# Optimization experiments

Hardware: AMD Instinct MI355X
Metric: run time of the kernel (lower is better)

Reference implementation:

```python
import jax, jax.numpy as jnp
import numpy as np

N_NODES = 100000
N_FEAT = 512
N_CLASS = 64
N_EDGES = 3200000
NLAYERS = 2


def setup_inputs() -> dict:
    key = jax.random.key(0)
    k1, k2, k3, k4, k5 = jax.random.split(key, 5)
    x = jax.random.normal(k1, (N_NODES, N_FEAT), dtype=jnp.float32)
    # xavier_uniform on weight.T => bound = sqrt(6/(fan_in+fan_out))
    bound = float(np.sqrt(6.0 / (N_FEAT + N_CLASS)))
    weight = jax.random.uniform(k2, (N_FEAT, N_CLASS), dtype=jnp.float32,
                                minval=-bound, maxval=bound)
    bias = jnp.zeros((N_CLASS,), dtype=jnp.float32)
    edge_row = jax.random.randint(k3, (N_EDGES,), 0, N_NODES, dtype=jnp.int32)
    edge_col = jax.random.randint(k4, (N_EDGES,), 0, N_NODES, dtype=jnp.int32)
    edge_val = jax.random.uniform(k5, (N_EDGES,), dtype=jnp.float32)
    return {"x": x, "weight": weight, "bias": bias,
            "edge_row": edge_row, "edge_col": edge_col, "edge_val": edge_val,
            "nlayers": NLAYERS}


def _spmm(edge_row, edge_col, edge_val, h):
    # out[r] = sum_{e: row[e]==r} val[e] * h[col[e]]   (adj @ h)
    msgs = edge_val[:, None] * h[edge_col]  # [E, C]
    return jax.ops.segment_sum(msgs, edge_row, num_segments=h.shape[0])


def reference(x, weight, bias, edge_row, edge_col, edge_val, nlayers):
    h = x @ weight                      # [N, C] dense GEMM
    for _ in range(nlayers):            # repeated sparse propagation
        h = _spmm(edge_row, edge_col, edge_val, h)
    h = h + bias
    return jax.nn.log_softmax(h, axis=1)
```

## Files before the change

### kernel.cpp

```cpp
#include <hip/hip_runtime.h>
#include <hip/hip_bf16.h>

constexpr int NROWS = 100000;
constexpr int K     = 512;
constexpr int C     = 64;
constexpr int E     = 3200000;

constexpr int NBK     = 256;
constexpr int BROWS   = 391;
constexpr int BSTRIDE = 13824;
constexpr int CHUNK   = 4096;

__global__ __launch_bounds__(256) void gemm64(const float* __restrict__ x,
                                              const float* __restrict__ w,
                                              float* __restrict__ h) {
  __shared__ float xs[128][65];
  __shared__ float ws[64][64];
  const int t    = threadIdx.x;
  const int cg   = (t & 15) * 4;
  const int rg   = (t >> 4) * 8;
  const int row0 = blockIdx.x * 128;

  float acc[8][4] = {};

  for (int k0 = 0; k0 < K; k0 += 64) {
    {
      const float4* wg  = (const float4*)(w + (size_t)k0 * C);
      float4*       wsv = (float4*)&ws[0][0];
#pragma unroll
      for (int i = 0; i < 4; ++i) wsv[t + 256 * i] = wg[t + 256 * i];
    }
#pragma unroll
    for (int i = 0; i < 8; ++i) {
      int idx = t + 256 * i;
      int r   = idx >> 4;
      int kk  = (idx & 15) * 4;
      int gr  = row0 + r;
      if (gr >= NROWS) gr = NROWS - 1;
      float4 v = *(const float4*)(x + (size_t)gr * K + k0 + kk);
      xs[r][kk]     = v.x;
      xs[r][kk + 1] = v.y;
      xs[r][kk + 2] = v.z;
      xs[r][kk + 3] = v.w;
    }
    __syncthreads();

#pragma unroll 8
    for (int kk = 0; kk < 64; ++kk) {
      float4 wv = *(const float4*)&ws[kk][cg];
      float xr[8];
#pragma unroll
      for (int i = 0; i < 8; ++i) xr[i] = xs[rg + i][kk];
#pragma unroll
      for (int i = 0; i < 8; ++i) {
        acc[i][0] += xr[i] * wv.x;
        acc[i][1] += xr[i] * wv.y;
        acc[i][2] += xr[i] * wv.z;
        acc[i][3] += xr[i] * wv.w;
      }
    }
    __syncthreads();
  }

#pragma unroll
  for (int i = 0; i < 8; ++i) {
    int gr = row0 + rg + i;
    if (gr < NROWS) {
      float4 v = {acc[i][0], acc[i][1], acc[i][2], acc[i][3]};
      *(float4*)(h + (size_t)gr * C + cg) = v;
    }
  }
}

__global__ __launch_bounds__(256) void init_bcur(int* __restrict__ bcur) {
  int t = threadIdx.x;
  if (t < NBK) bcur[t] = t * BSTRIDE;
}

__device__ inline int wave_incl_scan(int v, int lane) {
#pragma unroll
  for (int off = 1; off < 64; off <<= 1) {
    int t = __shfl_up(v, off, 64);
    if (lane >= off) v += t;
  }
  return v;
}

__global__ __launch_bounds__(256) void bin_by_row(const int* __restrict__ row,
                                                  const int* __restrict__ col,
                                                  const float* __restrict__ val,
                                                  int* bcur,
                                                  int2* __restrict__ binned) {
  __shared__ int hist[NBK];
  __shared__ int hcur[NBK];
  __shared__ int gbase[NBK];
  __shared__ int wt[4];
  __shared__ int2 lrec[CHUNK];
  __shared__ unsigned char lb[CHUNK];

  const int t  = threadIdx.x;
  const int e0 = blockIdx.x * CHUNK;
  const int n  = min(CHUNK, E - e0);

  hist[t] = 0;
  __syncthreads();

  int pb[16], px[16], pv[16];
#pragma unroll
  for (int i = 0; i < 16; ++i) {
    int e = e0 + 256 * i + t;
    pb[i] = -1;
    if (e < E) {
      int r = __builtin_nontemporal_load(row + e);
      int c = __builtin_nontemporal_load(col + e);
      float v = __builtin_nontemporal_load(val + e);
      int b = r / BROWS;
      pb[i] = b;
      px[i] = (r - b * BROWS) | (c << 9);
      pv[i] = __float_as_int(v);
      atomicAdd(&hist[b], 1);
    }
  }
  __syncthreads();

  {
    int lane = t & 63, wv = t >> 6;
    int d = hist[t];
    int inc = wave_incl_scan(d, lane);
    if (lane == 63) wt[wv] = inc;
    __syncthreads();
    int woff = 0;
    for (int w = 0; w < wv; ++w) woff += wt[w];
    hcur[t] = woff + inc - d;
  }

  {
    int cnt = hist[t];
    int gb  = cnt ? atomicAdd(&bcur[t], cnt) : 0;
    gbase[t] = gb - hcur[t];
  }
  __syncthreads();

#pragma unroll
  for (int i = 0; i < 16; ++i) {
    if (pb[i] >= 0) {
      int l = atomicAdd(&hcur[pb[i]], 1);
      lrec[l] = make_int2(px[i], pv[i]);
      lb[l]   = (unsigned char)pb[i];
    }
  }
  __syncthreads();

  for (int l = t; l < n; l += 256) {
    int b = lb[l];
    binned[gbase[b] + l] = lrec[l];
  }
}

__global__ __launch_bounds__(1024) void sort_bucket(const int2* __restrict__ binned,
                                                    const int* __restrict__ bcur,
                                                    int2* __restrict__ pack,
                                                    int* __restrict__ rs,
                                                    int* __restrict__ deg) {
  __shared__ int2 rec[BSTRIDE];
  __shared__ int  hist[BROWS];
  __shared__ int  excl[BROWS];
  __shared__ int  wt[16];

  const int b    = blockIdx.x;
  const int t    = threadIdx.x;
  const int base = b * BSTRIDE;
  const int cnt  = bcur[b] - base;

  for (int i = t; i < cnt; i += 1024) rec[i] = binned[base + i];
  for (int i = t; i < BROWS; i += 1024) hist[i] = 0;
  __syncthreads();

  for (int i = t; i < cnt; i += 1024) atomicAdd(&hist[rec[i].x & 511], 1);
  __syncthreads();

  {
    int lane = t & 63, wv = t >> 6;
    int d = (t < BROWS) ? hist[t] : 0;
    int inc = wave_incl_scan(d, lane);
    if (lane == 63) wt[wv] = inc;
    __syncthreads();
    int woff = 0;
    for (int w = 0; w < wv; ++w) woff += wt[w];
    if (t < BROWS) excl[t] = woff + inc - d;
  }
  __syncthreads();

  const int row0 = b * BROWS;
  for (int i = t; i < BROWS; i += 1024) {
    int gr = row0 + i;
    if (gr < NROWS) {
      rs[gr]  = base + excl[i];
      deg[gr] = hist[i];
    }
  }
  __syncthreads();

  for (int i = t; i < cnt; i += 1024) {
    int2 p    = rec[i];
    int local = p.x & 511;
    int off   = atomicAdd(&excl[local], 1);
    pack[base + off] = make_int2(((unsigned)p.x) >> 9, p.y);
  }
}

__global__ __launch_bounds__(256) void spmm_pull(const int* __restrict__ rs,
                                                 const int* __restrict__ deg,
                                                 const int2* __restrict__ pack,
                                                 const float* __restrict__ hin,
                                                 float* __restrict__ hout) {
  int r = blockIdx.x * 4 + (threadIdx.x >> 6);
  if (r >= NROWS) return;
  int lane  = threadIdx.x & 63;
  int start = rs[r], end = start + deg[r];
  float acc = 0.f;
  for (int base = start; base < end; base += 64) {
    int idx = base + lane;
    int2 p  = (idx < end) ? pack[idx] : make_int2(0, 0);
    int n   = min(64, end - base);
    int nn  = (n + 3) & ~3;
    for (int j = 0; j < nn; j += 4) {
      int   c0 = __shfl(p.x, j, 64),     c1 = __shfl(p.x, j + 1, 64);
      int   c2 = __shfl(p.x, j + 2, 64), c3 = __shfl(p.x, j + 3, 64);
      float v0 = __int_as_float(__shfl(p.y, j, 64));
      float v1 = __int_as_float(__shfl(p.y, j + 1, 64));
      float v2 = __int_as_float(__shfl(p.y, j + 2, 64));
      float v3 = __int_as_float(__shfl(p.y, j + 3, 64));
      float g0 = hin[(size_t)c0 * C + lane];
      float g1 = hin[(size_t)c1 * C + lane];
      float g2 = hin[(size_t)c2 * C + lane];
      float g3 = hin[(size_t)c3 * C + lane];
      acc += v0 * g0; acc += v1 * g1; acc += v2 * g2; acc += v3 * g3;
    }
  }
  hout[(size_t)r * C + lane] = acc;
}

__global__ __launch_bounds__(256) void spmm_atomic(const int* __restrict__ row,
                                                   const int* __restrict__ col,
                                                   const float* __restrict__ val,
                                                   const float* __restrict__ hin,
                                                   float* hout) {
  int e = blockIdx.x * 4 + (threadIdx.x >> 6);
  if (e >= E) return;
  int   c  = threadIdx.x & 63;
  int   r  = row[e];
  int   cl = col[e];
  float v  = val[e];
  atomicAdd(&hout[(size_t)r * C + c], v * hin[(size_t)cl * C + c]);
}

__global__ __launch_bounds__(256) void bias_lsm(const float* __restrict__ h,
                                                const float* __restrict__ bias,
                                                float* __restrict__ out) {
  int r = blockIdx.x * 4 + (threadIdx.x >> 6);
  if (r >= NROWS) return;
  int   c = threadIdx.x & 63;
  float v = h[(size_t)r * C + c] + bias[c];

  float m = v;
#pragma unroll
  for (int off = 32; off; off >>= 1) m = fmaxf(m, __shfl_xor(m, off, 64));
  float ex = __expf(v - m);
  float s  = ex;
#pragma unroll
  for (int off = 32; off; off >>= 1) s += __shfl_xor(s, off, 64);

  out[(size_t)r * C + c] = v - m - __logf(s);
}

extern "C" void kernel_launch(void* const* d_in, const int* in_sizes, int n_in,
                              void* d_out, int out_size, void* d_ws, size_t ws_size,
                              hipStream_t stream) {
  const float* x    = (const float*)d_in[0];
  const float* w    = (const float*)d_in[1];
  const float* bias = (const float*)d_in[2];
  const int*   erow = (const int*)d_in[3];
  const int*   ecol = (const int*)d_in[4];
  const float* eval = (const float*)d_in[5];

  float* out = (float*)d_out;

  const size_t hbytes = (size_t)NROWS * C * sizeof(float);
  const size_t bbytes = (size_t)NBK * BSTRIDE * sizeof(int2);
  char* ws = (char*)d_ws;

  const int nblk_bin = (E + CHUNK - 1) / CHUNK;

  const size_t regA = (bbytes > hbytes) ? bbytes : hbytes;

  size_t need = regA + bbytes  + (size_t)NROWS * 8 + (size_t)NBK * 4 + 8192;

  if (ws_size >= need) {
    char* p = ws;
    char* regA_p = p;                 p += regA;
    int2*  pack  = (int2*)p;          p += bbytes;
    int*   rs    = (int*)p;           p += (size_t)NROWS * 4;
    int*   deg   = (int*)p;           p += (size_t)NROWS * 4;
    int*   bcur  = (int*)p;

    int2*  binned = (int2*)regA_p;
    float* h0     = (float*)regA_p;
    float* hA     = out;

    init_bcur<<<1, 256, 0, stream>>>(bcur);
    bin_by_row<<<nblk_bin, 256, 0, stream>>>(erow, ecol, eval, bcur, binned);
    sort_bucket<<<NBK, 1024, 0, stream>>>(binned, bcur, pack, rs, deg);

    gemm64<<<(NROWS + 127) / 128, 256, 0, stream>>>(x, w, h0);

    spmm_pull<<<(NROWS + 3) / 4, 256, 0, stream>>>(rs, deg, pack, h0, hA);
    spmm_pull<<<(NROWS + 3) / 4, 256, 0, stream>>>(rs, deg, pack, hA, h0);

    bias_lsm<<<(NROWS + 3) / 4, 256, 0, stream>>>(h0, bias, out);
  } else {
    float* h0 = (float*)ws;
    float* hA = out;
    gemm64<<<(NROWS + 127) / 128, 256, 0, stream>>>(x, w, h0);
    hipMemsetAsync(hA, 0, hbytes, stream);
    spmm_atomic<<<(E + 3) / 4, 256, 0, stream>>>(erow, ecol, eval, h0, hA);
    hipMemsetAsync(h0, 0, hbytes, stream);
    spmm_atomic<<<(E + 3) / 4, 256, 0, stream>>>(erow, ecol, eval, hA, h0);
    bias_lsm<<<(NROWS + 3) / 4, 256, 0, stream>>>(h0, bias, out);
  }
}
```

Baseline: 645.8 us.

## Replace FP32 SIMT GEMM with split-bf16 MFMA GEMM using prepacked weight fragments

Replaces the shared-memory FP32 GEMM with a matrix-core kernel. The weights are split into bf16 hi/lo parts and prepacked into MFMA fragment layout, and x is split on the fly. Three bf16 MFMAs per tile approximate FP32 precision. This targets the compute cost of the dense x@W stage, at the price of a small accuracy loss and an extra prep kernel. It also reads x directly from global memory without LDS staging.

```diff
diff --git a/kernel.cpp b/kernel.cpp
--- a/kernel.cpp
+++ b/kernel.cpp
@@ -10,6 +10,111 @@
 constexpr int BROWS   = 391;
 constexpr int BSTRIDE = 13824;
 constexpr int CHUNK   = 4096;
+
+typedef __attribute__((ext_vector_type(8))) short bf16x8;
+typedef __attribute__((ext_vector_type(4))) float f32x4;
+
+__global__ __launch_bounds__(256) void prep_w(const float* __restrict__ w,
+                                              unsigned short* __restrict__ wfrag) {
+  int idx = blockIdx.x * 256 + threadIdx.x;
+  if (idx >= K * C) return;
+  int k = idx >> 6, n = idx & 63;
+  float v = w[idx];
+  unsigned u = __float_as_uint(v);
+  unsigned short hi = (unsigned short)(u >> 16);
+  float rem = v - __uint_as_float(u & 0xFFFF0000u);
+  unsigned lu = __float_as_uint(rem);
+  unsigned short lo = (unsigned short)((lu + 0x7FFF + ((lu >> 16) & 1)) >> 16);
+  int ks = k >> 5, kr = k & 31, g = kr >> 3, j = kr & 7;
+  int lane = (g << 4) | (n & 15), nt = n >> 4;
+  size_t base = ((size_t)(ks * 4 + nt)) * 1024 + lane * 8 + j;
+  wfrag[base]       = hi;
+  wfrag[base + 512] = lo;
+}
+
+__device__ inline bf16x8 pack_bf16x8(unsigned p0, unsigned p1, unsigned p2, unsigned p3) {
+  union { int4 i; bf16x8 b; } u;
+  u.i = make_int4((int)p0, (int)p1, (int)p2, (int)p3);
+  return u.b;
+}
+
+__global__ __launch_bounds__(256) void gemm_mfma(const float* __restrict__ x,
+                                                 const unsigned short* __restrict__ wfrag,
+                                                 float* __restrict__ h) {
+  const int t    = threadIdx.x;
+  const int lane = t & 63;
+  const int lr   = lane & 15;
+  const int g    = lane >> 4;
+  const int row0 = blockIdx.x * 64 + (t >> 6) * 16;
+
+  int gr = row0 + lr;
+  if (gr >= NROWS) gr = NROWS - 1;
+  const float* xr = x + (size_t)gr * K;
+
+  f32x4 acc0 = {0.f, 0.f, 0.f, 0.f};
+  f32x4 acc1 = {0.f, 0.f, 0.f, 0.f};
+  f32x4 acc2 = {0.f, 0.f, 0.f, 0.f};
+  f32x4 acc3 = {0.f, 0.f, 0.f, 0.f};
+
+  for (int ks = 0; ks < K / 32; ++ks) {
+    const float* xp = xr + ks * 32 + g * 8;
+    float4 A0 = *(const float4*)xp;
+    float4 A1 = *(const float4*)(xp + 4);
+    unsigned u0 = __float_as_uint(A0.x), u1 = __float_as_uint(A0.y);
+    unsigned u2 = __float_as_uint(A0.z), u3 = __float_as_uint(A0.w);
+    unsigned u4 = __float_as_uint(A1.x), u5 = __float_as_uint(A1.y);
+    unsigned u6 = __float_as_uint(A1.z), u7 = __float_as_uint(A1.w);
+    bf16x8 ah = pack_bf16x8((u1 & 0xFFFF0000u) | (u0 >> 16),
+                            (u3 & 0xFFFF0000u) | (u2 >> 16),
+                            (u5 & 0xFFFF0000u) | (u4 >> 16),
+                            (u7 & 0xFFFF0000u) | (u6 >> 16));
+    float r0 = A0.x - __uint_as_float(u0 & 0xFFFF0000u);
+    float r1 = A0.y - __uint_as_float(u1 & 0xFFFF0000u);
+    float r2 = A0.z - __uint_as_float(u2 & 0xFFFF0000u);
+    float r3 = A0.w - __uint_as_float(u3 & 0xFFFF0000u);
+    float r4 = A1.x - __uint_as_float(u4 & 0xFFFF0000u);
+    float r5 = A1.y - __uint_as_float(u5 & 0xFFFF0000u);
+    float r6 = A1.z - __uint_as_float(u6 & 0xFFFF0000u);
+    float r7 = A1.w - __uint_as_float(u7 & 0xFFFF0000u);
+    unsigned l0 = __float_as_uint(r0), l1 = __float_as_uint(r1);
+    unsigned l2 = __float_as_uint(r2), l3 = __float_as_uint(r3);
+    unsigned l4 = __float_as_uint(r4), l5 = __float_as_uint(r5);
+    unsigned l6 = __float_as_uint(r6), l7 = __float_as_uint(r7);
+    l0 = (l0 + 0x7FFF + ((l0 >> 16) & 1)) >> 16;
+    l1 = (l1 + 0x7FFF + ((l1 >> 16) & 1)) >> 16;
+    l2 = (l2 + 0x7FFF + ((l2 >> 16) & 1)) >> 16;
+    l3 = (l3 + 0x7FFF + ((l3 >> 16) & 1)) >> 16;
+    l4 = (l4 + 0x7FFF + ((l4 >> 16) & 1)) >> 16;
+    l5 = (l5 + 0x7FFF + ((l5 >> 16) & 1)) >> 16;
+    l6 = (l6 + 0x7FFF + ((l6 >> 16) & 1)) >> 16;
+    l7 = (l7 + 0x7FFF + ((l7 >> 16) & 1)) >> 16;
+    bf16x8 al = pack_bf16x8((l1 << 16) | l0, (l3 << 16) | l2,
+                            (l5 << 16) | l4, (l7 << 16) | l6);
+
+    const unsigned short* wp = wfrag + (size_t)ks * 4096;
+#pragma unroll
+    for (int nt = 0; nt < 4; ++nt) {
+      bf16x8 bh = *(const bf16x8*)(wp + nt * 1024 + lane * 8);
+      bf16x8 bl = *(const bf16x8*)(wp + nt * 1024 + 512 + lane * 8);
+      f32x4& acc = (nt == 0) ? acc0 : (nt == 1) ? acc1 : (nt == 2) ? acc2 : acc3;
+      acc = __builtin_amdgcn_mfma_f32_16x16x32_bf16(ah, bh, acc, 0, 0, 0);
+      acc = __builtin_amdgcn_mfma_f32_16x16x32_bf16(al, bh, acc, 0, 0, 0);
+      acc = __builtin_amdgcn_mfma_f32_16x16x32_bf16(ah, bl, acc, 0, 0, 0);
+    }
+  }
+
+#pragma unroll
+  for (int i = 0; i < 4; ++i) {
+    int r = row0 + g * 4 + i;
+    if (r < NROWS) {
+      float* hp = h + (size_t)r * C + lr;
+      hp[0]  = acc0[i];
+      hp[16] = acc1[i];
+      hp[32] = acc2[i];
+      hp[48] = acc3[i];
+    }
+  }
+}
 
 __global__ __launch_bounds__(256) void gemm64(const float* __restrict__ x,
                                               const float* __restrict__ w,
@@ -288,13 +393,15 @@
 
   const size_t hbytes = (size_t)NROWS * C * sizeof(float);
   const size_t bbytes = (size_t)NBK * BSTRIDE * sizeof(int2);
+  const size_t wfbytes = (size_t)K * C * 2 * sizeof(unsigned short);
   char* ws = (char*)d_ws;
 
   const int nblk_bin = (E + CHUNK - 1) / CHUNK;
 
   const size_t regA = (bbytes > hbytes) ? bbytes : hbytes;
 
-  size_t need = regA + bbytes  + (size_t)NROWS * 8 + (size_t)NBK * 4 + 8192;
+  size_t need = regA + bbytes  + (size_t)NROWS * 8 + (size_t)NBK * 4
+              + wfbytes + 8192;
 
   if (ws_size >= need) {
     char* p = ws;
@@ -302,17 +409,20 @@
     int2*  pack  = (int2*)p;          p += bbytes;
     int*   rs    = (int*)p;           p += (size_t)NROWS * 4;
     int*   deg   = (int*)p;           p += (size_t)NROWS * 4;
-    int*   bcur  = (int*)p;
+    int*   bcur  = (int*)p;           p += (size_t)NBK * 4;
+    unsigned short* wfrag = (unsigned short*)p;
 
     int2*  binned = (int2*)regA_p;
     float* h0     = (float*)regA_p;
     float* hA     = out;
 
+    prep_w<<<(K * C + 255) / 256, 256, 0, stream>>>(w, wfrag);
+
     init_bcur<<<1, 256, 0, stream>>>(bcur);
     bin_by_row<<<nblk_bin, 256, 0, stream>>>(erow, ecol, eval, bcur, binned);
     sort_bucket<<<NBK, 1024, 0, stream>>>(binned, bcur, pack, rs, deg);
 
-    gemm64<<<(NROWS + 127) / 128, 256, 0, stream>>>(x, w, h0);
+    gemm_mfma<<<(NROWS + 63) / 64, 256, 0, stream>>>(x, wfrag, h0);
 
     spmm_pull<<<(NROWS + 3) / 4, 256, 0, stream>>>(rs, deg, pack, h0, hA);
     spmm_pull<<<(NROWS + 3) / 4, 256, 0, stream>>>(rs, deg, pack, hA, h0);
```

Result: faster. 612.8 us (-5.1%).
